# Optimization experiments

Measured on AMD Instinct MI355X. Metric: run time of the kernel, lower is better.

## Reference

```python
import jax, jax.numpy as jnp
import numpy as np

N, E = 32768, 524288
MUL = 32        # multiplicity of 0e and 1o in hidden irreps
N_ATTR = 4      # node attr scalars (species one-hot)
N_RAD = 8       # radial basis size
FC_H = 64       # radial MLP hidden width
AVG_NEIGH = 16.0
INV3 = 1.0 / np.sqrt(3.0)  # w3j(1,1,0) contraction coefficient


def setup_inputs() -> dict:
    key = jax.random.key(0)
    ks = jax.random.split(key, 16)
    p = lambda k, s: jax.random.normal(k, s, dtype=jnp.float32)
    return {
        "node_feats": p(ks[0], (N, MUL + 3 * MUL)),
        "node_attrs": jax.random.uniform(ks[1], (N, N_ATTR), dtype=jnp.float32),
        "edge_feats": p(ks[2], (E, N_RAD)),
        "edge_attrs": p(ks[3], (E, 4)),
        "W1s": p(ks[4], (MUL, MUL)),
        "W1v": p(ks[5], (MUL, MUL)),
        "Wf1": p(ks[6], (N_RAD, FC_H)),
        "Wf2": p(ks[7], (FC_H, FC_H)),
        "Wf3": p(ks[8], (FC_H, 4 * MUL)),
        "W2s": p(ks[9], (2 * MUL, 2 * MUL)),
        "W2v": p(ks[10], (2 * MUL, MUL)),
        "Wsc_s": p(ks[11], (MUL, N_ATTR, 2 * MUL)),
        "Wsc_v": p(ks[12], (MUL, N_ATTR, MUL)),
        "edge_index": jax.random.randint(ks[13], (2, E), 0, N),
    }


def reference(node_feats, node_attrs, edge_feats, edge_attrs,
              W1s, W1v, Wf1, Wf2, Wf3, W2s, W2v, Wsc_s, Wsc_v, edge_index):
    silu = jax.nn.silu
    sender, receiver = edge_index[0], edge_index[1]
    xs0 = node_feats[:, :MUL]                      # [N, MUL]   0e scalars
    xv0 = node_feats[:, MUL:].reshape(-1, MUL, 3)  # [N, MUL, 3] 1o vectors

    # linear_1 (irrep-wise, e3nn fan-in normalization)
    xs = (xs0 @ W1s) / np.sqrt(MUL)
    xv = jnp.einsum('nui,uv->nvi', xv0, W1v) / np.sqrt(MUL)

    # radial MLP -> per-edge tensor-product weights
    h = silu((edge_feats @ Wf1) / np.sqrt(N_RAD))
    h = silu((h @ Wf2) / np.sqrt(FC_H))
    w = (h @ Wf3) / np.sqrt(FC_H)                  # [E, 4*MUL]
    w0, w1, w2, w3 = jnp.split(w, 4, axis=1)       # [E, MUL] each

    sh0 = edge_attrs[:, :1]                        # [E, 1]  l=0
    sh1 = edge_attrs[:, 1:4]                       # [E, 3]  l=1
    xs_e = xs[sender]                              # [E, MUL]
    xv_e = xv[sender]                              # [E, MUL, 3]

    # per-edge 'uvu' tensor product paths (only paths landing in 0e/1o kept)
    m_s0 = w0 * xs_e * sh0                                      # 0e x 0e -> 0e
    m_s1 = w3 * jnp.einsum('eui,ei->eu', xv_e, sh1) * INV3      # 1o x 1o -> 0e
    m_v0 = (w1 * xs_e)[:, :, None] * sh1[:, None, :]            # 0e x 1o -> 1o
    m_v1 = (w2 * sh0)[:, :, None] * xv_e                        # 1o x 0e -> 1o

    msg_s = jnp.concatenate([m_s0, m_s1], axis=1)               # [E, 2*MUL]
    msg_v = jnp.concatenate([m_v0, m_v1], axis=1)               # [E, 2*MUL, 3]

    # scatter-add message passing, normalized by avg num neighbours
    agg_s = jax.ops.segment_sum(msg_s, receiver, num_segments=N) / AVG_NEIGH
    agg_v = jax.ops.segment_sum(msg_v, receiver, num_segments=N) / AVG_NEIGH

    # linear_2 to conv output irreps (2*MUL x 0e + MUL x 1o)
    out_s = (agg_s @ W2s) / np.sqrt(2 * MUL)                    # [N, 2*MUL]
    out_v = jnp.einsum('nui,uv->nvi', agg_v, W2v) / np.sqrt(2 * MUL)

    # self connection: FullyConnectedTensorProduct(x_in, node_attrs)
    norm_sc = 1.0 / np.sqrt(MUL * N_ATTR)
    out_s = out_s + jnp.einsum('nu,na,uaw->nw', xs0, node_attrs, Wsc_s) * norm_sc
    out_v = out_v + jnp.einsum('nui,na,uaw->nwi', xv0, node_attrs, Wsc_v) * norm_sc

    # Gate nonlinearity: act(scalars) ++ act(gates) * gated vectors
    scalars = silu(out_s[:, :MUL])
    gates = silu(out_s[:, MUL:])
    gated = out_v * gates[:, :, None]
    new_feats = jnp.concatenate([scalars, gated.reshape(-1, 3 * MUL)], axis=1)

    # resnet add (irreps_layer_out == interaction_irreps_in)
    return node_feats + new_feats
```

## Files before the change

kernel.cpp:

```cpp
#include <hip/hip_runtime.h>
#include <hip/hip_bf16.h>

#define NN 32768
#define NE 524288

typedef __attribute__((ext_vector_type(8))) short short8v;
typedef __attribute__((ext_vector_type(4))) short short4v;
typedef __attribute__((ext_vector_type(4))) float f32x4;
typedef __attribute__((ext_vector_type(4))) float f32x4v;
typedef __attribute__((ext_vector_type(4))) unsigned u32x4;

__device__ __forceinline__ float silu_f(float x){ return x * (1.0f/(1.0f+__expf(-x))); }
__device__ __forceinline__ float bf2f(unsigned short u){ return __uint_as_float(((unsigned)u)<<16); }
__device__ __forceinline__ unsigned short f2bf(float f){
  __hip_bfloat16 b = __float2bfloat16(f);
  return __builtin_bit_cast(unsigned short, b);
}
__device__ __forceinline__ unsigned pk2(float lo, float hi){
  return (unsigned)f2bf(lo) | ((unsigned)f2bf(hi) << 16);
}

#define S32 0.17677669529663687f
#define S8  0.35355339059327373f
#define S64 0.125f
#define R16 0.0625f
#define NSC 0.08838834764831845f
#define INV3F 0.5773502691896258f

__global__ void k_zero(int* __restrict__ deg){
  deg[blockIdx.x*256 + threadIdx.x] = 0;
}

__global__ void k_hist(const int* __restrict__ eidx, int* __restrict__ deg){
  int e = blockIdx.x*256 + threadIdx.x;
  int r = eidx[NE + e];
  atomicAdd(&deg[r], 1);
}

__global__ void __launch_bounds__(1024) k_scan(const int* __restrict__ deg,
    int* __restrict__ row_start, int* __restrict__ cursor){
  __shared__ int lds[1024];
  int t = threadIdx.x;
  int4 v[8];
  const int4* dg = reinterpret_cast<const int4*>(deg) + t*8;
  int s = 0;
  #pragma unroll
  for (int j=0;j<8;j++){ v[j] = dg[j]; s += v[j].x+v[j].y+v[j].z+v[j].w; }
  lds[t] = s; __syncthreads();
  for (int off=1; off<1024; off<<=1){
    int q = (t>=off)? lds[t-off] : 0; __syncthreads();
    lds[t] += q; __syncthreads();
  }
  int run = (t==0)?0:lds[t-1];
  int4* rs = reinterpret_cast<int4*>(row_start) + t*8;
  int4* cu = reinterpret_cast<int4*>(cursor) + t*8;
  #pragma unroll
  for (int j=0;j<8;j++){
    int4 o;
    o.x = run; run += v[j].x;
    o.y = run; run += v[j].y;
    o.z = run; run += v[j].z;
    o.w = run; run += v[j].w;
    rs[j] = o; cu[j] = o;
  }
  if (t==1023) row_start[NN] = run;
}

__global__ void k_scatter(const int* __restrict__ eidx, int* __restrict__ cursor,
                          int* __restrict__ eperm, int* __restrict__ sperm){
  int e = blockIdx.x*256 + threadIdx.x;
  int r = eidx[NE + e];
  int s = eidx[e];
  int pos = atomicAdd(&cursor[r], 1);
  eperm[pos] = e;
  sperm[pos] = s;
}

#define XT_ITERS 16
__global__ void __launch_bounds__(256) k_xt(const float* __restrict__ nf,
    const float* __restrict__ W1s, const float* __restrict__ W1v,
    float* __restrict__ xtp2){
  __shared__ float rowbuf[256];
  int t = threadIdx.x;
  int c = t & 127, u = c >> 2, comp = c & 3;
  int node = t >> 7;
  const float* W = (comp==0) ? W1s : W1v;
  float wreg[32];
  #pragma unroll
  for (int k=0;k<32;k++) wreg[k] = W[k*32 + u];
  int soff = node*128 + (comp==0 ? 0 : 32 + (comp-1));
  int stride = (comp==0) ? 1 : 3;
  int base = blockIdx.x * (2*XT_ITERS);
  #pragma unroll 1
  for (int it=0; it<XT_ITERS; it++){
    int n0 = base + it*2;
    __syncthreads();
    rowbuf[t] = nf[(size_t)n0*128 + t];
    __syncthreads();
    float acc = 0.f;
    #pragma unroll
    for (int k=0;k<32;k++) acc += rowbuf[soff + k*stride] * wreg[k];
    xtp2[(size_t)(n0+node)*128 + c] = acc * S32;
  }
}

__global__ void k_wprep(const float* __restrict__ Wf1, const float* __restrict__ Wf2,
                        const float* __restrict__ Wf3,
                        const float* __restrict__ W2s, const float* __restrict__ W2v,
                        const float* __restrict__ Wsc_s, const float* __restrict__ Wsc_v,
                        short* __restrict__ wfrag, short* __restrict__ wfe){
  int f = blockIdx.x;
  int l = threadIdx.x;
  int c = l & 15, g = l >> 4;
  short8v pk;
  if (f < 28){
    #pragma unroll
    for (int j=0;j<8;j++){
      int k = ((j&4) ? 16 : 0) + g*4 + (j&3);
      float val;
      if (f < 4){
        int m = f;
        val = (k < 8) ? Wf1[k*64 + m*16 + c]*S8 : 0.f;
      } else if (f < 12){
        int idx = f-4, m = idx>>1, kk = idx&1;
        val = Wf2[(kk*32+k)*64 + m*16 + c]*S64;
      } else {
        int idx = f-12, m = idx>>1, kk = idx&1;
        val = Wf3[(kk*32+k)*128 + m*16 + c]*S64;
        if (m >= 6) val *= INV3F;
      }
      pk[j] = (short)f2bf(val);
    }
    reinterpret_cast<short8v*>(wfrag)[f*64 + l] = pk;
  } else {
    int fe = f - 28, kb = fe/6, p = fe%6;
    #pragma unroll
    for (int j=0;j<8;j++){
      int k = kb*32 + ((j&4) ? 16 : 0) + g*4 + (j&3);
      float val;
      if (p < 4){
        int col = p*16 + c;
        val = (k < 64) ? W2s[k*64 + col]*S64 : Wsc_s[(k-64)*64 + col]*NSC;
      } else {
        int col = (p-4)*16 + c;
        val = (k < 64) ? W2v[k*32 + col]*S64 : Wsc_v[(k-64)*32 + col]*NSC;
      }
      pk[j] = (short)f2bf(val);
    }
    reinterpret_cast<short8v*>(wfe)[fe*64 + l] = pk;
  }
}

__global__ void __launch_bounds__(256) k_mlp2(const float* __restrict__ ef,
    const float* __restrict__ ea, const int* __restrict__ eperm,
    const short* __restrict__ wfrag, unsigned* __restrict__ wpair,
    float* __restrict__ shp){
  int lane = threadIdx.x & 63;
  int wv = threadIdx.x >> 6;
  int tile = blockIdx.x*4 + wv;
  int e_l = lane & 15, g = lane >> 4;
  const short8v* wf = reinterpret_cast<const short8v*>(wfrag);

  int pos = tile*16 + e_l;
  int e = eperm[pos];
  if (lane < 16){
    f32x4v av = *reinterpret_cast<const f32x4v*>(ea + (size_t)e*4);
    __builtin_nontemporal_store(av, reinterpret_cast<f32x4v*>(shp + (size_t)pos*4));
  }

  short8v bx = {};
  if (lane < 32){
    const float4 xv = *reinterpret_cast<const float4*>(ef + (size_t)e*8 + g*4);
    bx[0]=(short)f2bf(xv.x); bx[1]=(short)f2bf(xv.y);
    bx[2]=(short)f2bf(xv.z); bx[3]=(short)f2bf(xv.w);
  }
  f32x4 a1[4];
  #pragma unroll
  for (int m=0;m<4;m++){
    f32x4 z = {};
    a1[m] = __builtin_amdgcn_mfma_f32_16x16x32_bf16(wf[m*64+lane], bx, z, 0,0,0);
  }
  short8v b2[2];
  #pragma unroll
  for (int m=0;m<4;m++)
    #pragma unroll
    for (int r=0;r<4;r++)
      b2[m>>1][(m&1)*4 + r] = (short)f2bf(silu_f(a1[m][r]));
  f32x4 a2[4] = {};
  #pragma unroll
  for (int kk=0;kk<2;kk++)
    #pragma unroll
    for (int m=0;m<4;m++)
      a2[m] = __builtin_amdgcn_mfma_f32_16x16x32_bf16(wf[(4+2*m+kk)*64+lane], b2[kk], a2[m], 0,0,0);
  short8v b3[2];
  #pragma unroll
  for (int m=0;m<4;m++)
    #pragma unroll
    for (int r=0;r<4;r++)
      b3[m>>1][(m&1)*4 + r] = (short)f2bf(silu_f(a2[m][r]));
  f32x4 a3[8] = {};
  #pragma unroll
  for (int kk=0;kk<2;kk++)
    #pragma unroll
    for (int m=0;m<8;m++)
      a3[m] = __builtin_amdgcn_mfma_f32_16x16x32_bf16(wf[(12+2*m+kk)*64+lane], b3[kk], a3[m], 0,0,0);
  unsigned* dst = wpair + (size_t)tile*1024 + e_l*64;
  #pragma unroll
  for (int mm=0; mm<2; mm++){
    u32x4 o;
    o.x = pk2(a3[mm][0], a3[mm+2][0]);
    o.y = pk2(a3[mm][1], a3[mm+2][1]);
    o.z = pk2(a3[mm][2], a3[mm+2][2]);
    o.w = pk2(a3[mm][3], a3[mm+2][3]);
    __builtin_nontemporal_store(o, reinterpret_cast<u32x4*>(dst + mm*16 + g*4));
    u32x4 o2;
    o2.x = pk2(a3[6+mm][0], a3[4+mm][0]);
    o2.y = pk2(a3[6+mm][1], a3[4+mm][1]);
    o2.z = pk2(a3[6+mm][2], a3[4+mm][2]);
    o2.w = pk2(a3[6+mm][3], a3[4+mm][3]);
    __builtin_nontemporal_store(o2, reinterpret_cast<u32x4*>(dst + 32 + mm*16 + g*4));
  }
}

__global__ void __launch_bounds__(256) k_recv(
    const float* __restrict__ shp, const int* __restrict__ row_start,
    const int* __restrict__ sperm, const unsigned* __restrict__ wpair,
    const float* __restrict__ xtp2, unsigned* __restrict__ agg){
  __shared__ float L[4][256];
  int wb = threadIdx.x >> 6;
  int lane = threadIdx.x & 63;
  int nl = wb >> 1, w = wb & 1;
  int n = blockIdx.x*2 + nl;
  int u = lane & 31;
  bool h1 = lane >= 32;

  int row = row_start[n], end = row_start[n+1];
  int mid = (row + end + 1) >> 1;
  int lo = w ? mid : row;
  int hi = w ? end : mid;

  float a0=0.f, a1=0.f, a2=0.f, a3=0.f;

#define EDGE_BODY(WP, SH, Q)                                         \
  {                                                                  \
    float wA = bf2f((unsigned short)((WP) & 0xffffu));               \
    float wB = bf2f((unsigned short)((WP) >> 16));                   \
    float x0 = h1 ? (Q).y : (Q).x;                                   \
    float x1 = h1 ? (Q).z : (Q).x;                                   \
    float x2 = h1 ? (Q).w : (Q).x;                                   \
    float c0 = h1 ? (SH).y : (SH).x;                                 \
    float c1 = h1 ? (SH).z : 0.f;                                    \
    float c2 = h1 ? (SH).w : 0.f;                                    \
    a0 += wA*(x0*c0 + x1*c1 + x2*c2);                                \
    float g0 = wB*(h1 ? (SH).x : (SH).y);                            \
    float g1 = wB*(h1 ? (SH).x : (SH).z);                            \
    float g2 = wB*(h1 ? (SH).x : (SH).w);                            \
    a1 += g0*x0; a2 += g1*x1; a3 += g2*x2;                           \
  }

  int idx = lo;
  for (; idx+4 <= hi; idx += 4){
    int s0 = sperm[idx+0], s1 = sperm[idx+1];
    int s2 = sperm[idx+2], s3 = sperm[idx+3];
    unsigned wp0 = __builtin_nontemporal_load(&wpair[(size_t)(idx+0)*64 + lane]);
    unsigned wp1 = __builtin_nontemporal_load(&wpair[(size_t)(idx+1)*64 + lane]);
    unsigned wp2 = __builtin_nontemporal_load(&wpair[(size_t)(idx+2)*64 + lane]);
    unsigned wp3 = __builtin_nontemporal_load(&wpair[(size_t)(idx+3)*64 + lane]);
    f32x4v sh0 = __builtin_nontemporal_load(reinterpret_cast<const f32x4v*>(shp + (size_t)(idx+0)*4));
    f32x4v sh1 = __builtin_nontemporal_load(reinterpret_cast<const f32x4v*>(shp + (size_t)(idx+1)*4));
    f32x4v sh2 = __builtin_nontemporal_load(reinterpret_cast<const f32x4v*>(shp + (size_t)(idx+2)*4));
    f32x4v sh3 = __builtin_nontemporal_load(reinterpret_cast<const f32x4v*>(shp + (size_t)(idx+3)*4));
    int b0 = __builtin_amdgcn_readfirstlane(s0);
    int b1 = __builtin_amdgcn_readfirstlane(s1);
    int b2 = __builtin_amdgcn_readfirstlane(s2);
    int b3 = __builtin_amdgcn_readfirstlane(s3);
    f32x4v q0 = *reinterpret_cast<const f32x4v*>(xtp2 + (size_t)b0*128 + u*4);
    f32x4v q1 = *reinterpret_cast<const f32x4v*>(xtp2 + (size_t)b1*128 + u*4);
    f32x4v q2 = *reinterpret_cast<const f32x4v*>(xtp2 + (size_t)b2*128 + u*4);
    f32x4v q3 = *reinterpret_cast<const f32x4v*>(xtp2 + (size_t)b3*128 + u*4);
    EDGE_BODY(wp0, sh0, q0);
    EDGE_BODY(wp1, sh1, q1);
    EDGE_BODY(wp2, sh2, q2);
    EDGE_BODY(wp3, sh3, q3);
  }
  for (; idx < hi; ++idx){
    int sb = __builtin_amdgcn_readfirstlane(sperm[idx]);
    unsigned wp = __builtin_nontemporal_load(&wpair[(size_t)idx*64 + lane]);
    f32x4v sh = __builtin_nontemporal_load(reinterpret_cast<const f32x4v*>(shp + (size_t)idx*4));
    f32x4v q = *reinterpret_cast<const f32x4v*>(xtp2 + (size_t)sb*128 + u*4);
    EDGE_BODY(wp, sh, q);
  }
#undef EDGE_BODY

  float* P = L[wb];
  P[lane] = a0; P[64+lane] = a1; P[128+lane] = a2; P[192+lane] = a3;
  __syncthreads();

  int t = threadIdx.x;
  int nl2 = t >> 7, cp = t & 127;
  float v0 = (L[nl2*2][2*cp  ] + L[nl2*2+1][2*cp  ]) * R16;
  float v1 = (L[nl2*2][2*cp+1] + L[nl2*2+1][2*cp+1]) * R16;
  agg[(size_t)(blockIdx.x*2 + nl2)*128 + cp] = pk2(v0, v1);
}

__global__ void __launch_bounds__(256) k_epi(
    const float* __restrict__ nf, const float* __restrict__ na,
    const unsigned short* __restrict__ agg, const short* __restrict__ wfe,
    float* __restrict__ out){
  __shared__ float L[4][16][168];
  int wv = threadIdx.x >> 6, lane = threadIdx.x & 63;
  int tile = blockIdx.x*4 + wv;
  int e = lane & 15, g = lane >> 4;
  int n = tile*16 + e;
  const short8v* WE = reinterpret_cast<const short8v*>(wfe);
  const unsigned short* ag = agg + (size_t)n*256;
  const float* nfr = nf + (size_t)n*128;
  float4 nav = *reinterpret_cast<const float4*>(na + (size_t)n*4);

  f32x4 as0={},as1={},as2={},as3={};
  f32x4 av00={},av01={},av10={},av11={},av20={},av21={};

  #pragma unroll
  for (int kb=0; kb<6; kb++){
    short8v bs, bv0, bv1, bv2;
    if (kb < 2){
      int k0 = kb*32 + g*4;
      #pragma unroll
      for (int i=0;i<4;i++){
        short4v qa = *reinterpret_cast<const short4v*>(ag + i*64 + k0);
        short4v qb = *reinterpret_cast<const short4v*>(ag + i*64 + k0 + 16);
        short8v b;
        b[0]=qa[0]; b[1]=qa[1]; b[2]=qa[2]; b[3]=qa[3];
        b[4]=qb[0]; b[5]=qb[1]; b[6]=qb[2]; b[7]=qb[3];
        if (i==0) bs = b; else if (i==1) bv0 = b; else if (i==2) bv1 = b; else bv2 = b;
      }
    } else {
      int u0 = (kb-2)*8 + g;
      float x0 = nfr[u0], x1 = nfr[u0+4];
      bs[0]=(short)f2bf(x0*nav.x); bs[1]=(short)f2bf(x0*nav.y);
      bs[2]=(short)f2bf(x0*nav.z); bs[3]=(short)f2bf(x0*nav.w);
      bs[4]=(short)f2bf(x1*nav.x); bs[5]=(short)f2bf(x1*nav.y);
      bs[6]=(short)f2bf(x1*nav.z); bs[7]=(short)f2bf(x1*nav.w);
      #pragma unroll
      for (int i=0;i<3;i++){
        float y0 = nfr[32 + u0*3 + i], y1 = nfr[32 + (u0+4)*3 + i];
        short8v b;
        b[0]=(short)f2bf(y0*nav.x); b[1]=(short)f2bf(y0*nav.y);
        b[2]=(short)f2bf(y0*nav.z); b[3]=(short)f2bf(y0*nav.w);
        b[4]=(short)f2bf(y1*nav.x); b[5]=(short)f2bf(y1*nav.y);
        b[6]=(short)f2bf(y1*nav.z); b[7]=(short)f2bf(y1*nav.w);
        if (i==0) bv0 = b; else if (i==1) bv1 = b; else bv2 = b;
      }
    }
    as0 = __builtin_amdgcn_mfma_f32_16x16x32_bf16(WE[(kb*6+0)*64+lane], bs, as0, 0,0,0);
    as1 = __builtin_amdgcn_mfma_f32_16x16x32_bf16(WE[(kb*6+1)*64+lane], bs, as1, 0,0,0);
    as2 = __builtin_amdgcn_mfma_f32_16x16x32_bf16(WE[(kb*6+2)*64+lane], bs, as2, 0,0,0);
    as3 = __builtin_amdgcn_mfma_f32_16x16x32_bf16(WE[(kb*6+3)*64+lane], bs, as3, 0,0,0);
    av00 = __builtin_amdgcn_mfma_f32_16x16x32_bf16(WE[(kb*6+4)*64+lane], bv0, av00, 0,0,0);
    av01 = __builtin_amdgcn_mfma_f32_16x16x32_bf16(WE[(kb*6+5)*64+lane], bv0, av01, 0,0,0);
    av10 = __builtin_amdgcn_mfma_f32_16x16x32_bf16(WE[(kb*6+4)*64+lane], bv1, av10, 0,0,0);
    av11 = __builtin_amdgcn_mfma_f32_16x16x32_bf16(WE[(kb*6+5)*64+lane], bv1, av11, 0,0,0);
    av20 = __builtin_amdgcn_mfma_f32_16x16x32_bf16(WE[(kb*6+4)*64+lane], bv2, av20, 0,0,0);
    av21 = __builtin_amdgcn_mfma_f32_16x16x32_bf16(WE[(kb*6+5)*64+lane], bv2, av21, 0,0,0);
  }

  float (*Lw)[168] = L[wv];
  #pragma unroll
  for (int r=0;r<4;r++){
    Lw[e][ 0 + g*4 + r] = silu_f(as0[r]);
    Lw[e][16 + g*4 + r] = silu_f(as1[r]);
    Lw[e][32 + g*4 + r] = silu_f(as2[r]);
    Lw[e][48 + g*4 + r] = silu_f(as3[r]);
    Lw[e][64 + (     g*4 + r)*3 + 0] = av00[r];
    Lw[e][64 + (16 + g*4 + r)*3 + 0] = av01[r];
    Lw[e][64 + (     g*4 + r)*3 + 1] = av10[r];
    Lw[e][64 + (16 + g*4 + r)*3 + 1] = av11[r];
    Lw[e][64 + (     g*4 + r)*3 + 2] = av20[r];
    Lw[e][64 + (16 + g*4 + r)*3 + 2] = av21[r];
  }
  __syncthreads();

  if (g == 0){
    #pragma unroll
    for (int c=0;c<32;c+=4){
      float4 nv = *reinterpret_cast<const float4*>(nfr + c);
      float4 o;
      o.x = nv.x + Lw[e][c  ];
      o.y = nv.y + Lw[e][c+1];
      o.z = nv.z + Lw[e][c+2];
      o.w = nv.w + Lw[e][c+3];
      *reinterpret_cast<float4*>(out + (size_t)n*128 + c) = o;
    }
  } else {
    int q0 = (g-1)*32;
    #pragma unroll
    for (int q=q0; q<q0+32; q+=4){
      float4 nv = *reinterpret_cast<const float4*>(nfr + 32 + q);
      float4 o;
      o.x = nv.x + Lw[e][64+q+0]*Lw[e][32+(q+0)/3];
      o.y = nv.y + Lw[e][64+q+1]*Lw[e][32+(q+1)/3];
      o.z = nv.z + Lw[e][64+q+2]*Lw[e][32+(q+2)/3];
      o.w = nv.w + Lw[e][64+q+3]*Lw[e][32+(q+3)/3];
      *reinterpret_cast<float4*>(out + (size_t)n*128 + 32 + q) = o;
    }
  }
}

extern "C" void kernel_launch(void* const* d_in, const int* in_sizes, int n_in,
                              void* d_out, int out_size, void* d_ws, size_t ws_size,
                              hipStream_t stream) {
  const float* nf    = (const float*)d_in[0];
  const float* na    = (const float*)d_in[1];
  const float* ef    = (const float*)d_in[2];
  const float* ea    = (const float*)d_in[3];
  const float* W1s   = (const float*)d_in[4];
  const float* W1v   = (const float*)d_in[5];
  const float* Wf1   = (const float*)d_in[6];
  const float* Wf2   = (const float*)d_in[7];
  const float* Wf3   = (const float*)d_in[8];
  const float* W2s   = (const float*)d_in[9];
  const float* W2v   = (const float*)d_in[10];
  const float* Wsc_s = (const float*)d_in[11];
  const float* Wsc_v = (const float*)d_in[12];
  const int*   eidx  = (const int*)d_in[13];
  float* out = (float*)d_out;

  char* ws = (char*)d_ws;
  size_t off = 0;
  auto alloc = [&](size_t bytes)->void*{
    void* p = ws + off; off += (bytes + 255) & ~(size_t)255; return p;
  };
  float*    xtp2      = (float*)alloc((size_t)NN*128*4);
  unsigned* wpair     = (unsigned*)alloc((size_t)NE*64*4);
  unsigned* agg       = (unsigned*)alloc((size_t)NN*256*2);
  float*    shp       = (float*)alloc((size_t)NE*16);
  int*      deg       = (int*)alloc((size_t)NN*4);
  int*      row_start = (int*)alloc((size_t)(NN+16)*4);
  int*      cursor    = (int*)alloc((size_t)NN*4);
  int*      eperm     = (int*)alloc((size_t)NE*4);
  int*      sperm     = (int*)alloc((size_t)NE*4);
  short*    wfrag     = (short*)alloc((size_t)28*64*8*2);
  short*    wfe       = (short*)alloc((size_t)36*64*8*2);
  if (off > ws_size) return;

  k_zero   <<<NN/256, 256, 0, stream>>>(deg);
  k_hist   <<<NE/256, 256, 0, stream>>>(eidx, deg);
  k_scan   <<<1, 1024, 0, stream>>>(deg, row_start, cursor);
  k_scatter<<<NE/256, 256, 0, stream>>>(eidx, cursor, eperm, sperm);
  k_xt     <<<NN/(2*XT_ITERS), 256, 0, stream>>>(nf, W1s, W1v, xtp2);
  k_wprep  <<<64, 64, 0, stream>>>(Wf1, Wf2, Wf3, W2s, W2v, Wsc_s, Wsc_v, wfrag, wfe);
  k_mlp2   <<<8192, 256, 0, stream>>>(ef, ea, eperm, wfrag, wpair, shp);
  k_recv   <<<NN/2, 256, 0, stream>>>(shp, row_start, sperm, wpair, xtp2,
                                      (unsigned*)agg);
  k_epi    <<<512, 256, 0, stream>>>(nf, na, (const unsigned short*)agg, wfe, out);
}
```

Before: 265.3 us.

## Assign whole receiver nodes per wavefront in k_recv, drop LDS reduction

The receiver aggregation kernel now gives each wavefront four consecutive receiver nodes, processed sequentially, instead of splitting one node's edge range across two wavefronts and combining the halves through shared memory with a block barrier. Lane pairs exchange their accumulators with a shuffle and even lanes write the packed bf16 results directly. This removes the LDS round trip and __syncthreads and cuts the grid size. In exchange each wave runs a longer serial chain of edges, which exposes load imbalance between nodes with different in-degrees and gives less parallelism to hide gather latency.

```diff
diff --git a/kernel.cpp b/kernel.cpp
--- a/kernel.cpp
+++ b/kernel.cpp
@@ -222,24 +222,17 @@
   }
 }
 
+#define RV_NODES 4
 __global__ void __launch_bounds__(256) k_recv(
     const float* __restrict__ shp, const int* __restrict__ row_start,
     const int* __restrict__ sperm, const unsigned* __restrict__ wpair,
     const float* __restrict__ xtp2, unsigned* __restrict__ agg){
-  __shared__ float L[4][256];
-  int wb = threadIdx.x >> 6;
+  int wv = threadIdx.x >> 6;
   int lane = threadIdx.x & 63;
-  int nl = wb >> 1, w = wb & 1;
-  int n = blockIdx.x*2 + nl;
   int u = lane & 31;
   bool h1 = lane >= 32;
-
-  int row = row_start[n], end = row_start[n+1];
-  int mid = (row + end + 1) >> 1;
-  int lo = w ? mid : row;
-  int hi = w ? end : mid;
-
-  float a0=0.f, a1=0.f, a2=0.f, a3=0.f;
+  bool even = (lane & 1) == 0;
+  int nbase = (blockIdx.x*4 + wv) * RV_NODES;
 
 #define EDGE_BODY(WP, SH, Q)                                         \
   {                                                                  \
@@ -258,49 +251,56 @@
     a1 += g0*x0; a2 += g1*x1; a3 += g2*x2;                           \
   }
 
-  int idx = lo;
-  for (; idx+4 <= hi; idx += 4){
-    int s0 = sperm[idx+0], s1 = sperm[idx+1];
-    int s2 = sperm[idx+2], s3 = sperm[idx+3];
-    unsigned wp0 = __builtin_nontemporal_load(&wpair[(size_t)(idx+0)*64 + lane]);
-    unsigned wp1 = __builtin_nontemporal_load(&wpair[(size_t)(idx+1)*64 + lane]);
-    unsigned wp2 = __builtin_nontemporal_load(&wpair[(size_t)(idx+2)*64 + lane]);
-    unsigned wp3 = __builtin_nontemporal_load(&wpair[(size_t)(idx+3)*64 + lane]);
-    f32x4v sh0 = __builtin_nontemporal_load(reinterpret_cast<const f32x4v*>(shp + (size_t)(idx+0)*4));
-    f32x4v sh1 = __builtin_nontemporal_load(reinterpret_cast<const f32x4v*>(shp + (size_t)(idx+1)*4));
-    f32x4v sh2 = __builtin_nontemporal_load(reinterpret_cast<const f32x4v*>(shp + (size_t)(idx+2)*4));
-    f32x4v sh3 = __builtin_nontemporal_load(reinterpret_cast<const f32x4v*>(shp + (size_t)(idx+3)*4));
-    int b0 = __builtin_amdgcn_readfirstlane(s0);
-    int b1 = __builtin_amdgcn_readfirstlane(s1);
-    int b2 = __builtin_amdgcn_readfirstlane(s2);
-    int b3 = __builtin_amdgcn_readfirstlane(s3);
-    f32x4v q0 = *reinterpret_cast<const f32x4v*>(xtp2 + (size_t)b0*128 + u*4);
-    f32x4v q1 = *reinterpret_cast<const f32x4v*>(xtp2 + (size_t)b1*128 + u*4);
-    f32x4v q2 = *reinterpret_cast<const f32x4v*>(xtp2 + (size_t)b2*128 + u*4);
-    f32x4v q3 = *reinterpret_cast<const f32x4v*>(xtp2 + (size_t)b3*128 + u*4);
-    EDGE_BODY(wp0, sh0, q0);
-    EDGE_BODY(wp1, sh1, q1);
-    EDGE_BODY(wp2, sh2, q2);
-    EDGE_BODY(wp3, sh3, q3);
-  }
-  for (; idx < hi; ++idx){
-    int sb = __builtin_amdgcn_readfirstlane(sperm[idx]);
-    unsigned wp = __builtin_nontemporal_load(&wpair[(size_t)idx*64 + lane]);
-    f32x4v sh = __builtin_nontemporal_load(reinterpret_cast<const f32x4v*>(shp + (size_t)idx*4));
-    f32x4v q = *reinterpret_cast<const f32x4v*>(xtp2 + (size_t)sb*128 + u*4);
-    EDGE_BODY(wp, sh, q);
+  #pragma unroll 1
+  for (int nn=0; nn<RV_NODES; nn++){
+    int n = nbase + nn;
+    int lo = row_start[n], hi = row_start[n+1];
+    float a0=0.f, a1=0.f, a2=0.f, a3=0.f;
+    int idx = lo;
+    for (; idx+4 <= hi; idx += 4){
+      int s0 = sperm[idx+0], s1 = sperm[idx+1];
+      int s2 = sperm[idx+2], s3 = sperm[idx+3];
+      unsigned wp0 = __builtin_nontemporal_load(&wpair[(size_t)(idx+0)*64 + lane]);
+      unsigned wp1 = __builtin_nontemporal_load(&wpair[(size_t)(idx+1)*64 + lane]);
+      unsigned wp2 = __builtin_nontemporal_load(&wpair[(size_t)(idx+2)*64 + lane]);
+      unsigned wp3 = __builtin_nontemporal_load(&wpair[(size_t)(idx+3)*64 + lane]);
+      f32x4v sh0 = __builtin_nontemporal_load(reinterpret_cast<const f32x4v*>(shp + (size_t)(idx+0)*4));
+      f32x4v sh1 = __builtin_nontemporal_load(reinterpret_cast<const f32x4v*>(shp + (size_t)(idx+1)*4));
+      f32x4v sh2 = __builtin_nontemporal_load(reinterpret_cast<const f32x4v*>(shp + (size_t)(idx+2)*4));
+      f32x4v sh3 = __builtin_nontemporal_load(reinterpret_cast<const f32x4v*>(shp + (size_t)(idx+3)*4));
+      int b0 = __builtin_amdgcn_readfirstlane(s0);
+      int b1 = __builtin_amdgcn_readfirstlane(s1);
+      int b2 = __builtin_amdgcn_readfirstlane(s2);
+      int b3 = __builtin_amdgcn_readfirstlane(s3);
+      f32x4v q0 = *reinterpret_cast<const f32x4v*>(xtp2 + (size_t)b0*128 + u*4);
+      f32x4v q1 = *reinterpret_cast<const f32x4v*>(xtp2 + (size_t)b1*128 + u*4);
+      f32x4v q2 = *reinterpret_cast<const f32x4v*>(xtp2 + (size_t)b2*128 + u*4);
+      f32x4v q3 = *reinterpret_cast<const f32x4v*>(xtp2 + (size_t)b3*128 + u*4);
+      EDGE_BODY(wp0, sh0, q0);
+      EDGE_BODY(wp1, sh1, q1);
+      EDGE_BODY(wp2, sh2, q2);
+      EDGE_BODY(wp3, sh3, q3);
+    }
+    for (; idx < hi; ++idx){
+      int sb = __builtin_amdgcn_readfirstlane(sperm[idx]);
+      unsigned wp = __builtin_nontemporal_load(&wpair[(size_t)idx*64 + lane]);
+      f32x4v sh = __builtin_nontemporal_load(reinterpret_cast<const f32x4v*>(shp + (size_t)idx*4));
+      f32x4v q = *reinterpret_cast<const f32x4v*>(xtp2 + (size_t)sb*128 + u*4);
+      EDGE_BODY(wp, sh, q);
+    }
+    float p0 = __shfl_xor(a0, 1);
+    float p1 = __shfl_xor(a1, 1);
+    float p2 = __shfl_xor(a2, 1);
+    float p3 = __shfl_xor(a3, 1);
+    if (even){
+      unsigned* ag = agg + (size_t)n*128 + (lane>>1);
+      ag[0]  = pk2(a0*R16, p0*R16);
+      ag[32] = pk2(a1*R16, p1*R16);
+      ag[64] = pk2(a2*R16, p2*R16);
+      ag[96] = pk2(a3*R16, p3*R16);
+    }
   }
 #undef EDGE_BODY
-
-  float* P = L[wb];
-  P[lane] = a0; P[64+lane] = a1; P[128+lane] = a2; P[192+lane] = a3;
-  __syncthreads();
-
-  int t = threadIdx.x;
-  int nl2 = t >> 7, cp = t & 127;
-  float v0 = (L[nl2*2][2*cp  ] + L[nl2*2+1][2*cp  ]) * R16;
-  float v1 = (L[nl2*2][2*cp+1] + L[nl2*2+1][2*cp+1]) * R16;
-  agg[(size_t)(blockIdx.x*2 + nl2)*128 + cp] = pk2(v0, v1);
 }
 
 __global__ void __launch_bounds__(256) k_epi(
@@ -450,7 +450,7 @@
   k_xt     <<<NN/(2*XT_ITERS), 256, 0, stream>>>(nf, W1s, W1v, xtp2);
   k_wprep  <<<64, 64, 0, stream>>>(Wf1, Wf2, Wf3, W2s, W2v, Wsc_s, Wsc_v, wfrag, wfe);
   k_mlp2   <<<8192, 256, 0, stream>>>(ef, ea, eperm, wfrag, wpair, shp);
-  k_recv   <<<NN/2, 256, 0, stream>>>(shp, row_start, sperm, wpair, xtp2,
+  k_recv   <<<NN/(4*RV_NODES), 256, 0, stream>>>(shp, row_start, sperm, wpair, xtp2,
                                       (unsigned*)agg);
   k_epi    <<<512, 256, 0, stream>>>(nf, na, (const unsigned short*)agg, wfe, out);
 }
```

New measurement: 254.8 us. 4.0% less time.
